# Performance work log

Hardware: AMD Instinct MI355X
Metric: run time of the kernel (lower is better)

The kernel has to match this reference:

```python
import jax, jax.numpy as jnp
import numpy as np

NUM_CLS = 80
C = 256
IMG = 1024.0
N = 256
SR = 2  # sampling_ratio
MIN_SIZE = 16.0
SCALES = (0.25, 0.125, 0.0625, 0.03125)
HW = ((256, 256), (128, 128), (64, 64), (32, 32))


def _roialign(feat, rois, scale, out):
    # feat: [C, H, W]; rois: [n, 4] (y1, x1, y2, x2) in image coords.
    # torchvision-style ROIAlign (aligned=False), sampling_ratio=SR, avg pool.
    Cc, H, W = feat.shape
    n = rois.shape[0]
    y1 = rois[:, 0] * scale
    x1 = rois[:, 1] * scale
    rh = jnp.maximum(rois[:, 2] * scale - y1, 1.0)
    rw = jnp.maximum(rois[:, 3] * scale - x1, 1.0)
    # per-bin sample offsets: (bin + (s+0.5)/SR) * bin_size
    g = (jnp.arange(out, dtype=feat.dtype)[:, None]
         + (jnp.arange(SR, dtype=feat.dtype)[None, :] + 0.5) / SR).reshape(-1)  # [out*SR]
    ys = y1[:, None] + g[None, :] * (rh / out)[:, None]  # [n, out*SR]
    xs = x1[:, None] + g[None, :] * (rw / out)[:, None]
    S = out * SR
    yy = jnp.broadcast_to(ys[:, :, None], (n, S, S)).reshape(n, S * S)
    xx = jnp.broadcast_to(xs[:, None, :], (n, S, S)).reshape(n, S * S)
    valid = (yy > -1.0) & (yy < H) & (xx > -1.0) & (xx < W)
    yc = jnp.clip(yy, 0.0, H - 1.0)
    xc = jnp.clip(xx, 0.0, W - 1.0)
    y0 = jnp.floor(yc)
    x0 = jnp.floor(xc)
    ly = yc - y0
    lx = xc - x0
    y0i = y0.astype(jnp.int32)
    x0i = x0.astype(jnp.int32)
    y1i = jnp.minimum(y0i + 1, H - 1)
    x1i = jnp.minimum(x0i + 1, W - 1)
    f00 = feat[:, y0i, x0i]  # [C, n, S*S]
    f01 = feat[:, y0i, x1i]
    f10 = feat[:, y1i, x0i]
    f11 = feat[:, y1i, x1i]
    val = (f00 * (1 - ly) * (1 - lx) + f01 * (1 - ly) * lx
           + f10 * ly * (1 - lx) + f11 * ly * lx)
    val = jnp.where(valid[None], val, 0.0)
    val = val.reshape(Cc, n, out, SR, out, SR).mean(axis=(3, 5))
    return val.transpose(1, 0, 2, 3)  # [n, C, out, out]


def _pool(P, rois, out):
    # roi_layer: FPN level assignment via log2 of sqrt(area)/224, clamp to levels 0..3
    area = jnp.prod(rois[:, 2:4] - rois[:, 0:2] + 1.0, axis=-1)
    lvl = jnp.clip(jnp.floor(4.0 + jnp.log(jnp.sqrt(area) / 224.0) / np.log(2.0)), 2.0, 5.0) - 2.0
    lvl = lvl.astype(jnp.int32)
    pooled = jnp.zeros((rois.shape[0], C, out, out), dtype=rois.dtype)
    for l in range(4):
        pl = _roialign(P[l], rois, SCALES[l], out)
        pooled = pooled + jnp.where((lvl == l)[:, None, None, None], pl, 0.0)
    return pooled


def _loc2bbox(loc, anchor):
    chw = anchor[..., 2:4] - anchor[..., 0:2]
    cyx = anchor[..., 0:2] + chw * 0.5
    yx = loc[..., 0:2] * chw + cyx
    hw = jnp.exp(loc[..., 2:4]) * chw
    return jnp.concatenate([yx - hw * 0.5, yx + hw * 0.5], axis=-1)


def _head(x, W1, b1, W2, b2, Wc, bc, Wl, bl):
    x = x.reshape(x.shape[0], -1)
    h = jax.nn.relu(x @ W1 + b1)
    h = jax.nn.relu(h @ W2 + b2)
    return h @ Wc + bc, h @ Wl + bl


def _cascade(P, rois, params):
    stds = (jnp.array([0.1, 0.1, 0.2, 0.2], dtype=rois.dtype),
            jnp.array([0.05, 0.05, 0.1, 0.1], dtype=rois.dtype),
            jnp.array([1 / 30.0, 1 / 30.0, 1 / 15.0, 1 / 15.0], dtype=rois.dtype))
    roi = rois
    valid = jnp.ones((rois.shape[0],), dtype=bool)
    t = jnp.arange(rois.shape[0])
    pre_b = jnp.zeros((rois.shape[0], NUM_CLS, 4), dtype=rois.dtype)
    pre_s = jnp.zeros((rois.shape[0], NUM_CLS), dtype=rois.dtype)
    for s in range(3):
        x = _pool(P, roi, 7)
        logits, loc = _head(x, *params[s])
        loc = loc.reshape(-1, NUM_CLS + 1, 4)[:, 1:] * stds[s]
        boxes = _loc2bbox(loc, roi[:, None, :])  # [N, NUM_CLS, 4]
        score = jax.nn.softmax(logits, axis=-1)[:, 1:]
        pre_b = pre_b + boxes
        pre_s = pre_s + score
        best = jnp.argmax(score, axis=-1)
        roi = boxes[t, best]
        roi = jnp.clip(roi, 0.0, IMG)  # square image: clamp both coords to [0, IMG]
        if s < 2:  # original filters only after stages 1 and 2
            hw = roi[:, 2:4] - roi[:, 0:2]
            valid = valid & jnp.all(hw >= MIN_SIZE, axis=-1)
    m = valid.astype(pre_s.dtype)
    return pre_b / 3.0 * m[:, None, None], pre_s / 3.0 * m[:, None]


def setup_inputs():
    key = jax.random.key(0)
    ks = jax.random.split(key, 32)
    inp = {}
    for i, (h, w) in enumerate(HW):
        inp[f"P{i}"] = jax.random.normal(ks[i], (C, h, w), dtype=jnp.float32)
    yx1 = jax.random.uniform(ks[4], (N, 2), minval=0.0, maxval=IMG - 64.0)
    sz = jnp.exp(jax.random.uniform(ks[5], (N, 2), minval=np.log(16.0), maxval=np.log(600.0)))
    yx2 = jnp.clip(yx1 + sz, 0.0, IMG - 1.0)
    inp["rois"] = jnp.concatenate([yx1, yx2], axis=-1).astype(jnp.float32)
    dims = [(C * 49, 1024), (1024,), (1024, 1024), (1024,),
            (1024, NUM_CLS + 1), (NUM_CLS + 1,), (1024, (NUM_CLS + 1) * 4), ((NUM_CLS + 1) * 4,)]
    names = ["W1", "b1", "W2", "b2", "Wc", "bc", "Wl", "bl"]
    k = 6
    for s in range(3):
        for nm, d in zip(names, dims):
            if len(d) == 1:
                inp[f"s{s}_{nm}"] = jnp.zeros(d, dtype=jnp.float32)
            else:
                inp[f"s{s}_{nm}"] = 0.02 * jax.random.normal(ks[k], d, dtype=jnp.float32)
                k += 1
    return inp


def reference(P0, P1, P2, P3, rois,
              s0_W1, s0_b1, s0_W2, s0_b2, s0_Wc, s0_bc, s0_Wl, s0_bl,
              s1_W1, s1_b1, s1_W2, s1_b2, s1_Wc, s1_bc, s1_Wl, s1_bl,
              s2_W1, s2_b1, s2_W2, s2_b2, s2_Wc, s2_bc, s2_Wl, s2_bl):
    P = (P0, P1, P2, P3)
    params = [(s0_W1, s0_b1, s0_W2, s0_b2, s0_Wc, s0_bc, s0_Wl, s0_bl),
              (s1_W1, s1_b1, s1_W2, s1_b2, s1_Wc, s1_bc, s1_Wl, s1_bl),
              (s2_W1, s2_b1, s2_W2, s2_b2, s2_Wc, s2_bc, s2_Wl, s2_bl)]
    return _cascade(P, rois, params)
```

## Files before the change

### kernel.cpp

```cpp
#include <hip/hip_runtime.h>
#include <math.h>


#define NROI 256
#define NCLS 80
#define APITCH 40

typedef __attribute__((ext_vector_type(8))) short short8;
typedef __attribute__((ext_vector_type(4))) float f32x4;

struct __attribute__((aligned(8))) US4 { unsigned short a, b, c, d; };

__device__ __forceinline__ unsigned short f2bf(float f) {
  unsigned u = __builtin_bit_cast(unsigned, f);
  unsigned r = (u + 0x7FFFu + ((u >> 16) & 1u)) >> 16;
  return (unsigned short)r;
}
__device__ __forceinline__ float bf2f(unsigned short u) {
  return __builtin_bit_cast(float, (unsigned)u << 16);
}

struct PrepArgs {
  const float* W1[3];
  const float* W2[3];
  const float* Wc[3];
  const float* Wl[3];
  unsigned short* Wt1[3];
  unsigned short* Wt2[3];
  unsigned short* Wth[3];
  const float* rois;
  float* roi;
  float* valid;
  float* zero_base;
  int zero_count;
};

__global__ __launch_bounds__(256) void prep_all(PrepArgs a) {
  __shared__ unsigned short tile[32][33];
  const int b = blockIdx.x;
  const int t = threadIdx.x;
  const int r = t >> 3;
  const int c4 = (t & 7) * 4;

  if (b < 37632) {
    int s = b / 12544;
    int tau = b % 12544;
    int kd0 = (tau % 392) * 32;
    int n0 = (tau / 392) * 32;
    int p = kd0 >> 8;
    int c0 = kd0 & 255;
    int k_src = (c0 + r) * 49 + p;
    float4 v = *(const float4*)(a.W1[s] + (size_t)k_src * 1024 + n0 + c4);
    tile[r][c4 + 0] = f2bf(v.x);
    tile[r][c4 + 1] = f2bf(v.y);
    tile[r][c4 + 2] = f2bf(v.z);
    tile[r][c4 + 3] = f2bf(v.w);
    __syncthreads();
    US4 o = {tile[c4 + 0][r], tile[c4 + 1][r], tile[c4 + 2][r], tile[c4 + 3][r]};
    *(US4*)(a.Wt1[s] + (size_t)(n0 + r) * 12544 + kd0 + c4) = o;
  } else if (b < 40704) {
    int bb = b - 37632;
    int s = bb / 1024;
    int tau = bb % 1024;
    int k0 = (tau % 32) * 32;
    int n0 = (tau / 32) * 32;
    float4 v = *(const float4*)(a.W2[s] + (size_t)(k0 + r) * 1024 + n0 + c4);
    tile[r][c4 + 0] = f2bf(v.x);
    tile[r][c4 + 1] = f2bf(v.y);
    tile[r][c4 + 2] = f2bf(v.z);
    tile[r][c4 + 3] = f2bf(v.w);
    __syncthreads();
    US4 o = {tile[c4 + 0][r], tile[c4 + 1][r], tile[c4 + 2][r], tile[c4 + 3][r]};
    *(US4*)(a.Wt2[s] + (size_t)(n0 + r) * 1024 + k0 + c4) = o;
  } else if (b < 42240) {
    int bb = b - 40704;
    int s = bb / 512;
    int tau = bb % 512;
    int k0 = (tau % 32) * 32;
    int n0 = (tau / 32) * 32;
#pragma unroll
    for (int j = 0; j < 4; j++) {
      int nn = n0 + c4 + j;
      float v = 0.0f;
      if (nn < 81) v = a.Wc[s][(size_t)(k0 + r) * 81 + nn];
      else if (nn < 405) v = a.Wl[s][(size_t)(k0 + r) * 324 + (nn - 81)];
      tile[r][c4 + j] = f2bf(v);
    }
    __syncthreads();
    US4 o = {tile[c4 + 0][r], tile[c4 + 1][r], tile[c4 + 2][r], tile[c4 + 3][r]};
    *(US4*)(a.Wth[s] + (size_t)(n0 + r) * 1024 + k0 + c4) = o;
  } else if (b == 42240) {
    for (int i = t; i < NROI * 4; i += 256) a.roi[i] = a.rois[i];
    a.valid[t] = 1.0f;
  } else {
    int base = (b - 42241) * 1024 + t;
#pragma unroll
    for (int j = 0; j < 4; j++) {
      int ii = base + j * 256;
      if (ii < a.zero_count) a.zero_base[ii] = 0.0f;
    }
  }
}

__global__ __launch_bounds__(256) void feat_all(
    const float* __restrict__ P0, const float* __restrict__ P1,
    const float* __restrict__ P2, const float* __restrict__ P3,
    unsigned short* __restrict__ Pb0, unsigned short* __restrict__ Pb1,
    unsigned short* __restrict__ Pb2, unsigned short* __restrict__ Pb3) {
  __shared__ unsigned short tile[32][33];
  const int b = blockIdx.x;
  const int t = threadIdx.x;
  const float* src;
  unsigned short* dst;
  int N, tau;
  if (b < 16384)      { src = P0; dst = Pb0; N = 65536; tau = b; }
  else if (b < 20480) { src = P1; dst = Pb1; N = 16384; tau = b - 16384; }
  else if (b < 21504) { src = P2; dst = Pb2; N = 4096;  tau = b - 20480; }
  else                { src = P3; dst = Pb3; N = 1024;  tau = b - 21504; }
  int k0 = (tau & 7) * 32;
  int n0 = (tau >> 3) * 32;
  int r = t >> 3;
  int c4 = (t & 7) * 4;
  float4 v = *(const float4*)(src + (size_t)(k0 + r) * N + n0 + c4);
  tile[r][c4 + 0] = f2bf(v.x);
  tile[r][c4 + 1] = f2bf(v.y);
  tile[r][c4 + 2] = f2bf(v.z);
  tile[r][c4 + 3] = f2bf(v.w);
  __syncthreads();
  US4 o = {tile[c4 + 0][r], tile[c4 + 1][r], tile[c4 + 2][r], tile[c4 + 3][r]};
  *(US4*)(dst + (size_t)(n0 + r) * 256 + k0 + c4) = o;
}

__global__ __launch_bounds__(256) void pool_kernel2(
    const unsigned short* __restrict__ Pb0, const unsigned short* __restrict__ Pb1,
    const unsigned short* __restrict__ Pb2, const unsigned short* __restrict__ Pb3,
    const float* __restrict__ roi, unsigned short* __restrict__ pooled) {
  int t = threadIdx.x;
  int n = blockIdx.y;
  int p = blockIdx.x * 4 + (t >> 6);
  if (p >= 49) return;
  int lane = t & 63;
  int c4 = lane * 4;
  int py = p / 7, px = p % 7;

  float r0 = roi[n * 4 + 0];
  float r1 = roi[n * 4 + 1];
  float r2 = roi[n * 4 + 2];
  float r3 = roi[n * 4 + 3];

  float area = (r2 - r0 + 1.0f) * (r3 - r1 + 1.0f);
  float lf = floorf(4.0f + log2f(sqrtf(area) / 224.0f));
  lf = fminf(fmaxf(lf, 2.0f), 5.0f);
  int lvl = (int)lf - 2;

  float scale;
  int H;
  const unsigned short* fb;
  if (lvl == 0)      { scale = 0.25f;    H = 256; fb = Pb0; }
  else if (lvl == 1) { scale = 0.125f;   H = 128; fb = Pb1; }
  else if (lvl == 2) { scale = 0.0625f;  H = 64;  fb = Pb2; }
  else               { scale = 0.03125f; H = 32;  fb = Pb3; }
  int W = H;

  float y1 = r0 * scale;
  float x1 = r1 * scale;
  float rh = fmaxf(r2 * scale - y1, 1.0f);
  float rw = fmaxf(r3 * scale - x1, 1.0f);
  float bh = rh * (1.0f / 7.0f);
  float bw = rw * (1.0f / 7.0f);

  float a0 = 0.f, a1 = 0.f, a2 = 0.f, a3 = 0.f;
#pragma unroll
  for (int ry = 0; ry < 2; ry++) {
    float yy = y1 + ((float)py + ((float)ry + 0.5f) * 0.5f) * bh;
    bool vy = (yy > -1.0f) && (yy < (float)H);
    float ycl = fminf(fmaxf(yy, 0.0f), (float)(H - 1));
    float y0f = floorf(ycl);
    float ly = ycl - y0f;
    int y0i = (int)y0f;
    int y1i = min(y0i + 1, H - 1);
#pragma unroll
    for (int rx = 0; rx < 2; rx++) {
      float xx = x1 + ((float)px + ((float)rx + 0.5f) * 0.5f) * bw;
      bool vx = (xx > -1.0f) && (xx < (float)W);
      float xcl = fminf(fmaxf(xx, 0.0f), (float)(W - 1));
      float x0f = floorf(xcl);
      float lx = xcl - x0f;
      int x0i = (int)x0f;
      int x1i = min(x0i + 1, W - 1);
      float w00 = (1.f - ly) * (1.f - lx);
      float w01 = (1.f - ly) * lx;
      float w10 = ly * (1.f - lx);
      float w11 = ly * lx;
      if (!(vy && vx)) { w00 = w01 = w10 = w11 = 0.f; }
      ushort4 f00 = *(const ushort4*)(fb + ((size_t)(y0i * W + x0i) * 256 + c4));
      ushort4 f01 = *(const ushort4*)(fb + ((size_t)(y0i * W + x1i) * 256 + c4));
      ushort4 f10 = *(const ushort4*)(fb + ((size_t)(y1i * W + x0i) * 256 + c4));
      ushort4 f11 = *(const ushort4*)(fb + ((size_t)(y1i * W + x1i) * 256 + c4));
      a0 += bf2f(f00.x) * w00 + bf2f(f01.x) * w01 + bf2f(f10.x) * w10 + bf2f(f11.x) * w11;
      a1 += bf2f(f00.y) * w00 + bf2f(f01.y) * w01 + bf2f(f10.y) * w10 + bf2f(f11.y) * w11;
      a2 += bf2f(f00.z) * w00 + bf2f(f01.z) * w01 + bf2f(f10.z) * w10 + bf2f(f11.z) * w11;
      a3 += bf2f(f00.w) * w00 + bf2f(f01.w) * w01 + bf2f(f10.w) * w10 + bf2f(f11.w) * w11;
    }
  }
  ushort4 o;
  o.x = f2bf(a0 * 0.25f);
  o.y = f2bf(a1 * 0.25f);
  o.z = f2bf(a2 * 0.25f);
  o.w = f2bf(a3 * 0.25f);
  *(ushort4*)(pooled + (size_t)n * 12544 + p * 256 + c4) = o;
}

__global__ __launch_bounds__(256) void gemm_bf16(
    const unsigned short* __restrict__ A, const unsigned short* __restrict__ B,
    float* __restrict__ Cpart, int M, int N, int K, int iters,
    const float* __restrict__ bias, unsigned short* __restrict__ fused_out) {
  __shared__ unsigned short As[128 * APITCH];
  __shared__ unsigned short Bs[128 * APITCH];
  const int t = threadIdx.x;
  const int n0 = blockIdx.x * 128;
  const int m0 = blockIdx.y * 128;
  const size_t kt0 = (size_t)blockIdx.z * iters * 32;

  const int row = t >> 2;
  const int off = (t & 3) * 8;
  const unsigned short* pa0 = A + (size_t)(m0 + row) * K + kt0 + off;
  const unsigned short* pa1 = pa0 + (size_t)64 * K;
  const unsigned short* pb0 = B + (size_t)(n0 + row) * K + kt0 + off;
  const unsigned short* pb1 = pb0 + (size_t)64 * K;

  const int lane = t & 63;
  const int wave = t >> 6;
  const int wm = (wave >> 1) * 64;
  const int wn = (wave & 1) * 64;
  const int fr = lane & 15;
  const int kq = (lane >> 4) * 8;

  f32x4 acc[4][4];
#pragma unroll
  for (int i = 0; i < 4; i++)
#pragma unroll
    for (int j = 0; j < 4; j++) acc[i][j] = (f32x4){0.f, 0.f, 0.f, 0.f};

  uint4 ra0 = *(const uint4*)pa0;
  uint4 ra1 = *(const uint4*)pa1;
  uint4 rb0 = *(const uint4*)pb0;
  uint4 rb1 = *(const uint4*)pb1;

  for (int it = 0; it < iters; ++it) {
    *(uint4*)&As[row * APITCH + off] = ra0;
    *(uint4*)&As[(row + 64) * APITCH + off] = ra1;
    *(uint4*)&Bs[row * APITCH + off] = rb0;
    *(uint4*)&Bs[(row + 64) * APITCH + off] = rb1;
    __syncthreads();
    if (it + 1 < iters) {
      int d = (it + 1) * 32;
      ra0 = *(const uint4*)(pa0 + d);
      ra1 = *(const uint4*)(pa1 + d);
      rb0 = *(const uint4*)(pb0 + d);
      rb1 = *(const uint4*)(pb1 + d);
    }
    short8 af[4], bfv[4];
#pragma unroll
    for (int f = 0; f < 4; f++)
      af[f] = *(const short8*)&As[(wm + f * 16 + fr) * APITCH + kq];
#pragma unroll
    for (int f = 0; f < 4; f++)
      bfv[f] = *(const short8*)&Bs[(wn + f * 16 + fr) * APITCH + kq];
#pragma unroll
    for (int fm = 0; fm < 4; fm++)
#pragma unroll
      for (int fn = 0; fn < 4; fn++)
        acc[fm][fn] = __builtin_amdgcn_mfma_f32_16x16x32_bf16(af[fm], bfv[fn],
                                                              acc[fm][fn], 0, 0, 0);
    __syncthreads();
  }

  const int colb = n0 + wn + fr;
  const int rowb = m0 + wm + (lane >> 4) * 4;
  if (fused_out) {
#pragma unroll
    for (int fm = 0; fm < 4; fm++)
#pragma unroll
      for (int fn = 0; fn < 4; fn++) {
        int col = colb + fn * 16;
        float bv = bias[col];
#pragma unroll
        for (int r = 0; r < 4; r++) {
          float v = fmaxf(acc[fm][fn][r] + bv, 0.0f);
          fused_out[(size_t)(rowb + fm * 16 + r) * N + col] = f2bf(v);
        }
      }
  } else {
    float* Cp = Cpart + (size_t)blockIdx.z * M * N;
#pragma unroll
    for (int fm = 0; fm < 4; fm++)
#pragma unroll
      for (int fn = 0; fn < 4; fn++)
#pragma unroll
        for (int r = 0; r < 4; r++)
          Cp[(size_t)(rowb + fm * 16 + r) * N + (colb + fn * 16)] = acc[fm][fn][r];
  }
}

__global__ __launch_bounds__(256) void reduce_bias_relu(
    const float* __restrict__ parts, int nparts, const float* __restrict__ bias,
    unsigned short* __restrict__ outb) {
  int i = blockIdx.x * 256 + threadIdx.x;
  float s = 0.0f;
  for (int p = 0; p < nparts; ++p) s += parts[(size_t)p * 262144 + i];
  s = fmaxf(s + bias[i & 1023], 0.0f);
  outb[i] = f2bf(s);
}

__global__ __launch_bounds__(128) void decode_kernel(
    const float* __restrict__ headp, const float* __restrict__ bc,
    const float* __restrict__ bl,
    float* __restrict__ roi, float* __restrict__ valid,
    float* __restrict__ pre_b, float* __restrict__ pre_s,
    float st0, float st1, float st2, float st3, int stage) {
  int n = blockIdx.x;
  int t = threadIdx.x;
  __shared__ float red[128];
  __shared__ int redi[128];
  __shared__ float sroi[4];
  __shared__ float boxes[NCLS][4];

  if (t < 4) sroi[t] = roi[n * 4 + t];
  float l = -INFINITY;
  if (t < 81) {
    float s = 0.f;
#pragma unroll
    for (int z = 0; z < 4; z++) s += headp[(size_t)z * 131072 + n * 512 + t];
    l = s + bc[t];
  }
  red[t] = l;
  __syncthreads();
#pragma unroll
  for (int s = 64; s > 0; s >>= 1) {
    if (t < s) red[t] = fmaxf(red[t], red[t + s]);
    __syncthreads();
  }
  float mx = red[0];
  __syncthreads();
  red[t] = (t < 81) ? expf(l - mx) : 0.0f;
  __syncthreads();
#pragma unroll
  for (int s = 64; s > 0; s >>= 1) {
    if (t < s) red[t] += red[t + s];
    __syncthreads();
  }
  float denom = red[0];
  __syncthreads();

  float score = -INFINITY;
  if (t < NCLS) {
    float lj = 0.f;
#pragma unroll
    for (int z = 0; z < 4; z++) lj += headp[(size_t)z * 131072 + n * 512 + (t + 1)];
    lj += bc[t + 1];
    score = expf(lj - mx) / denom;
    float lp[4];
#pragma unroll
    for (int j = 0; j < 4; j++) {
      float s = 0.f;
#pragma unroll
      for (int z = 0; z < 4; z++)
        s += headp[(size_t)z * 131072 + n * 512 + 81 + (t + 1) * 4 + j];
      lp[j] = s + bl[(t + 1) * 4 + j];
    }
    float dy = lp[0] * st0;
    float dx = lp[1] * st1;
    float dh = lp[2] * st2;
    float dw = lp[3] * st3;
    float h_ = sroi[2] - sroi[0];
    float w_ = sroi[3] - sroi[1];
    float cy = sroi[0] + h_ * 0.5f;
    float cx = sroi[1] + w_ * 0.5f;
    float ny = dy * h_ + cy;
    float nx = dx * w_ + cx;
    float nh = expf(dh) * h_;
    float nw = expf(dw) * w_;
    float b0 = ny - nh * 0.5f;
    float b1v = nx - nw * 0.5f;
    float b2v = ny + nh * 0.5f;
    float b3v = nx + nw * 0.5f;
    int o = (n * NCLS + t) * 4;
    pre_b[o + 0] += b0;
    pre_b[o + 1] += b1v;
    pre_b[o + 2] += b2v;
    pre_b[o + 3] += b3v;
    pre_s[n * NCLS + t] += score;
    boxes[t][0] = b0;
    boxes[t][1] = b1v;
    boxes[t][2] = b2v;
    boxes[t][3] = b3v;
  }
  red[t] = score;
  redi[t] = t;
  __syncthreads();
  for (int s = 64; s > 0; s >>= 1) {
    if (t < s) {
      float o2 = red[t + s];
      int oi = redi[t + s];
      if (o2 > red[t] || (o2 == red[t] && oi < redi[t])) {
        red[t] = o2;
        redi[t] = oi;
      }
    }
    __syncthreads();
  }
  if (t == 0) {
    int best = redi[0];
    float ry1 = fminf(fmaxf(boxes[best][0], 0.0f), 1024.0f);
    float rx1 = fminf(fmaxf(boxes[best][1], 0.0f), 1024.0f);
    float ry2 = fminf(fmaxf(boxes[best][2], 0.0f), 1024.0f);
    float rx2 = fminf(fmaxf(boxes[best][3], 0.0f), 1024.0f);
    roi[n * 4 + 0] = ry1;
    roi[n * 4 + 1] = rx1;
    roi[n * 4 + 2] = ry2;
    roi[n * 4 + 3] = rx2;
    if (stage < 2) {
      float hh = ry2 - ry1, ww = rx2 - rx1;
      if (!(hh >= 16.0f && ww >= 16.0f)) valid[n] = 0.0f;
    }
  }
}

__global__ __launch_bounds__(256) void finalize_kernel(
    const float* __restrict__ pre_b, const float* __restrict__ pre_s,
    const float* __restrict__ valid, float* __restrict__ out) {
  int i = blockIdx.x * 256 + threadIdx.x;
  if (i < NROI * NCLS * 4) {
    int n = i / (NCLS * 4);
    out[i] = pre_b[i] * valid[n] * (1.0f / 3.0f);
  } else if (i < NROI * NCLS * 4 + NROI * NCLS) {
    int j = i - NROI * NCLS * 4;
    int n = j / NCLS;
    out[i] = pre_s[j] * valid[n] * (1.0f / 3.0f);
  }
}

extern "C" void kernel_launch(void* const* d_in, const int* in_sizes, int n_in,
                              void* d_out, int out_size, void* d_ws, size_t ws_size,
                              hipStream_t stream) {
  const float* P0 = (const float*)d_in[0];
  const float* P1 = (const float*)d_in[1];
  const float* P2 = (const float*)d_in[2];
  const float* P3 = (const float*)d_in[3];
  const float* rois = (const float*)d_in[4];
  float* out = (float*)d_out;
  float* ws = (float*)d_ws;

  float* roi   = ws;
  float* valid = roi + 1024;
  float* pre_b = valid + 256;
  float* pre_s = pre_b + 81920;
  float* part1 = pre_s + 20480;
  float* parth = part1 + 14 * 262144;
  unsigned short* pooledb = (unsigned short*)(parth + 4 * 131072);
  unsigned short* Wt1s = pooledb + (size_t)256 * 12544;
  unsigned short* Wt2s = Wt1s + (size_t)3 * 1024 * 12544;
  unsigned short* Wths = Wt2s + (size_t)3 * 1024 * 1024;
  unsigned short* h1b = Wths + (size_t)3 * 512 * 1024;
  unsigned short* h2b = h1b + (size_t)256 * 1024;
  unsigned short* Pb0 = h2b + (size_t)256 * 1024;
  unsigned short* Pb1 = Pb0 + (size_t)65536 * 256;
  unsigned short* Pb2 = Pb1 + (size_t)16384 * 256;
  unsigned short* Pb3 = Pb2 + (size_t)4096 * 256;

  PrepArgs pa;
  for (int s = 0; s < 3; s++) {
    pa.W1[s] = (const float*)d_in[5 + s * 8 + 0];
    pa.W2[s] = (const float*)d_in[5 + s * 8 + 2];
    pa.Wc[s] = (const float*)d_in[5 + s * 8 + 4];
    pa.Wl[s] = (const float*)d_in[5 + s * 8 + 6];
    pa.Wt1[s] = Wt1s + (size_t)s * 1024 * 12544;
    pa.Wt2[s] = Wt2s + (size_t)s * 1024 * 1024;
    pa.Wth[s] = Wths + (size_t)s * 512 * 1024;
  }
  pa.rois = rois;
  pa.roi = roi;
  pa.valid = valid;
  pa.zero_base = pre_b;
  pa.zero_count = 81920 + 20480;

  feat_all<<<21760, 256, 0, stream>>>(P0, P1, P2, P3, Pb0, Pb1, Pb2, Pb3);
  prep_all<<<42341, 256, 0, stream>>>(pa);

  const float stds[3][4] = {
      {0.1f, 0.1f, 0.2f, 0.2f},
      {0.05f, 0.05f, 0.1f, 0.1f},
      {1.0f / 30.0f, 1.0f / 30.0f, 1.0f / 15.0f, 1.0f / 15.0f}};

  for (int s = 0; s < 3; s++) {
    const float* b1 = (const float*)d_in[5 + s * 8 + 1];
    const float* b2 = (const float*)d_in[5 + s * 8 + 3];
    const float* bc = (const float*)d_in[5 + s * 8 + 5];
    const float* bl = (const float*)d_in[5 + s * 8 + 7];

    pool_kernel2<<<dim3(13, 256), 256, 0, stream>>>(Pb0, Pb1, Pb2, Pb3, roi, pooledb);

    gemm_bf16<<<dim3(8, 2, 14), 256, 0, stream>>>(
        pooledb, pa.Wt1[s], part1, 256, 1024, 12544, 28, nullptr, nullptr);
    reduce_bias_relu<<<1024, 256, 0, stream>>>(part1, 14, b1, h1b);

    gemm_bf16<<<dim3(8, 2, 1), 256, 0, stream>>>(
        h1b, pa.Wt2[s], nullptr, 256, 1024, 1024, 32, b2, h2b);

    gemm_bf16<<<dim3(4, 2, 4), 256, 0, stream>>>(
        h2b, pa.Wth[s], parth, 256, 512, 1024, 8, nullptr, nullptr);

    decode_kernel<<<256, 128, 0, stream>>>(parth, bc, bl, roi, valid, pre_b, pre_s,
                                           stds[s][0], stds[s][1], stds[s][2], stds[s][3], s);
  }

  finalize_kernel<<<400, 256, 0, stream>>>(pre_b, pre_s, valid, out);
}
```

Measured before the change: 516.9 us.

## Merge feature/weight transposes into one kernel with larger tiles; split-K second GEMM

Folds the feature-map bf16 transpose into the weight prep kernel and moves from 32x32 to 64x256 tiles. Each thread now writes wide 16-byte rows and launches far fewer blocks, cutting per-block overhead and improving write coalescing. The second FC GEMM changes from a single-slice fused bias/ReLU epilogue running on 16 blocks to an 8-way split-K (128 blocks) followed by a separate reduce kernel. This trades extra partial-sum traffic and one more launch per stage for more parallelism.

```diff
diff --git a/kernel.cpp b/kernel.cpp
--- a/kernel.cpp
+++ b/kernel.cpp
@@ -5,11 +5,10 @@
 #define NROI 256
 #define NCLS 80
 #define APITCH 40
+#define TP 264
 
 typedef __attribute__((ext_vector_type(8))) short short8;
 typedef __attribute__((ext_vector_type(4))) float f32x4;
-
-struct __attribute__((aligned(8))) US4 { unsigned short a, b, c, d; };
 
 __device__ __forceinline__ unsigned short f2bf(float f) {
   unsigned u = __builtin_bit_cast(unsigned, f);
@@ -28,6 +27,8 @@
   unsigned short* Wt1[3];
   unsigned short* Wt2[3];
   unsigned short* Wth[3];
+  const float* P[4];
+  unsigned short* Pb[4];
   const float* rois;
   float* roi;
   float* valid;
@@ -36,99 +37,111 @@
 };
 
 __global__ __launch_bounds__(256) void prep_all(PrepArgs a) {
-  __shared__ unsigned short tile[32][33];
+  __shared__ unsigned short tile[64 * TP];
   const int b = blockIdx.x;
   const int t = threadIdx.x;
-  const int r = t >> 3;
-  const int c4 = (t & 7) * 4;
-
-  if (b < 37632) {
-    int s = b / 12544;
-    int tau = b % 12544;
-    int kd0 = (tau % 392) * 32;
-    int n0 = (tau / 392) * 32;
-    int p = kd0 >> 8;
-    int c0 = kd0 & 255;
-    int k_src = (c0 + r) * 49 + p;
-    float4 v = *(const float4*)(a.W1[s] + (size_t)k_src * 1024 + n0 + c4);
-    tile[r][c4 + 0] = f2bf(v.x);
-    tile[r][c4 + 1] = f2bf(v.y);
-    tile[r][c4 + 2] = f2bf(v.z);
-    tile[r][c4 + 3] = f2bf(v.w);
-    __syncthreads();
-    US4 o = {tile[c4 + 0][r], tile[c4 + 1][r], tile[c4 + 2][r], tile[c4 + 3][r]};
-    *(US4*)(a.Wt1[s] + (size_t)(n0 + r) * 12544 + kd0 + c4) = o;
-  } else if (b < 40704) {
-    int bb = b - 37632;
-    int s = bb / 1024;
-    int tau = bb % 1024;
-    int k0 = (tau % 32) * 32;
-    int n0 = (tau / 32) * 32;
-    float4 v = *(const float4*)(a.W2[s] + (size_t)(k0 + r) * 1024 + n0 + c4);
-    tile[r][c4 + 0] = f2bf(v.x);
-    tile[r][c4 + 1] = f2bf(v.y);
-    tile[r][c4 + 2] = f2bf(v.z);
-    tile[r][c4 + 3] = f2bf(v.w);
-    __syncthreads();
-    US4 o = {tile[c4 + 0][r], tile[c4 + 1][r], tile[c4 + 2][r], tile[c4 + 3][r]};
-    *(US4*)(a.Wt2[s] + (size_t)(n0 + r) * 1024 + k0 + c4) = o;
-  } else if (b < 42240) {
-    int bb = b - 40704;
-    int s = bb / 512;
-    int tau = bb % 512;
-    int k0 = (tau % 32) * 32;
-    int n0 = (tau / 32) * 32;
-#pragma unroll
-    for (int j = 0; j < 4; j++) {
-      int nn = n0 + c4 + j;
-      float v = 0.0f;
-      if (nn < 81) v = a.Wc[s][(size_t)(k0 + r) * 81 + nn];
-      else if (nn < 405) v = a.Wl[s][(size_t)(k0 + r) * 324 + (nn - 81)];
-      tile[r][c4 + j] = f2bf(v);
-    }
-    __syncthreads();
-    US4 o = {tile[c4 + 0][r], tile[c4 + 1][r], tile[c4 + 2][r], tile[c4 + 3][r]};
-    *(US4*)(a.Wth[s] + (size_t)(n0 + r) * 1024 + k0 + c4) = o;
-  } else if (b == 42240) {
+
+  const float* src = nullptr;
+  unsigned short* dst = nullptr;
+  size_t srcN = 0, dstP = 0;
+  int k0 = 0, n0 = 0;
+  int mode = 0;
+  int hs = 0;
+
+  if (b < 2352) {
+    int s = b / 784, tau = b % 784;
+    int kd0 = (tau % 196) * 64;
+    n0 = (tau / 196) * 256;
+    src = a.W1[s]; srcN = 1024;
+    dst = a.Wt1[s]; dstP = 12544;
+    k0 = kd0; mode = 1;
+  } else if (b < 3712) {
+    int x = b - 2352;
+    int l, base;
+    if (x < 1024)      { l = 0; base = x; }
+    else if (x < 1280) { l = 1; base = x - 1024; }
+    else if (x < 1344) { l = 2; base = x - 1280; }
+    else               { l = 3; base = x - 1344; }
+    static const int NHW[4] = {65536, 16384, 4096, 1024};
+    src = a.P[l]; srcN = NHW[l];
+    dst = a.Pb[l]; dstP = 256;
+    k0 = (base & 3) * 64;
+    n0 = (base >> 2) * 256;
+  } else if (b < 3904) {
+    int x = b - 3712;
+    int s = x / 64, tau = x % 64;
+    src = a.W2[s]; srcN = 1024;
+    dst = a.Wt2[s]; dstP = 1024;
+    k0 = (tau % 16) * 64;
+    n0 = (tau / 16) * 256;
+  } else if (b < 4000) {
+    int x = b - 3904;
+    hs = x / 32;
+    int tau = x % 32;
+    dst = a.Wth[hs]; dstP = 1024;
+    k0 = (tau % 16) * 64;
+    n0 = (tau / 16) * 256;
+    mode = 2;
+  } else if (b == 4000) {
     for (int i = t; i < NROI * 4; i += 256) a.roi[i] = a.rois[i];
     a.valid[t] = 1.0f;
+    return;
   } else {
-    int base = (b - 42241) * 1024 + t;
+    int base = (b - 4001) * 1024 + t;
 #pragma unroll
     for (int j = 0; j < 4; j++) {
       int ii = base + j * 256;
       if (ii < a.zero_count) a.zero_base[ii] = 0.0f;
     }
-  }
-}
-
-__global__ __launch_bounds__(256) void feat_all(
-    const float* __restrict__ P0, const float* __restrict__ P1,
-    const float* __restrict__ P2, const float* __restrict__ P3,
-    unsigned short* __restrict__ Pb0, unsigned short* __restrict__ Pb1,
-    unsigned short* __restrict__ Pb2, unsigned short* __restrict__ Pb3) {
-  __shared__ unsigned short tile[32][33];
-  const int b = blockIdx.x;
-  const int t = threadIdx.x;
-  const float* src;
-  unsigned short* dst;
-  int N, tau;
-  if (b < 16384)      { src = P0; dst = Pb0; N = 65536; tau = b; }
-  else if (b < 20480) { src = P1; dst = Pb1; N = 16384; tau = b - 16384; }
-  else if (b < 21504) { src = P2; dst = Pb2; N = 4096;  tau = b - 20480; }
-  else                { src = P3; dst = Pb3; N = 1024;  tau = b - 21504; }
-  int k0 = (tau & 7) * 32;
-  int n0 = (tau >> 3) * 32;
-  int r = t >> 3;
-  int c4 = (t & 7) * 4;
-  float4 v = *(const float4*)(src + (size_t)(k0 + r) * N + n0 + c4);
-  tile[r][c4 + 0] = f2bf(v.x);
-  tile[r][c4 + 1] = f2bf(v.y);
-  tile[r][c4 + 2] = f2bf(v.z);
-  tile[r][c4 + 3] = f2bf(v.w);
+    return;
+  }
+
+  const int rp = t >> 6;
+  const int c4 = (t & 63) * 4;
+  if (mode == 2) {
+#pragma unroll 4
+    for (int pass = 0; pass < 16; pass++) {
+      int r = pass * 4 + rp;
+      int k = k0 + r;
+      unsigned short vv[4];
+#pragma unroll
+      for (int j = 0; j < 4; j++) {
+        int nn = n0 + c4 + j;
+        float v = 0.0f;
+        if (nn < 81) v = a.Wc[hs][(size_t)k * 81 + nn];
+        else if (nn < 405) v = a.Wl[hs][(size_t)k * 324 + (nn - 81)];
+        vv[j] = f2bf(v);
+      }
+      *(uint2*)&tile[r * TP + c4] =
+          (uint2){(unsigned)vv[0] | ((unsigned)vv[1] << 16),
+                  (unsigned)vv[2] | ((unsigned)vv[3] << 16)};
+    }
+  } else {
+    const int p_ = k0 >> 8;
+    const int c0_ = k0 & 255;
+#pragma unroll 4
+    for (int pass = 0; pass < 16; pass++) {
+      int r = pass * 4 + rp;
+      size_t ksrc = (mode == 1) ? ((size_t)(c0_ + r) * 49 + p_) : (size_t)(k0 + r);
+      float4 v = *(const float4*)(src + ksrc * srcN + n0 + c4);
+      *(uint2*)&tile[r * TP + c4] =
+          (uint2){(unsigned)f2bf(v.x) | ((unsigned)f2bf(v.y) << 16),
+                  (unsigned)f2bf(v.z) | ((unsigned)f2bf(v.w) << 16)};
+    }
+  }
   __syncthreads();
-  US4 o = {tile[c4 + 0][r], tile[c4 + 1][r], tile[c4 + 2][r], tile[c4 + 3][r]};
-  *(US4*)(dst + (size_t)(n0 + r) * 256 + k0 + c4) = o;
+
+  unsigned w[32];
+#pragma unroll
+  for (int i = 0; i < 32; i++) {
+    unsigned lo = tile[(2 * i) * TP + t];
+    unsigned hi = tile[(2 * i + 1) * TP + t];
+    w[i] = lo | (hi << 16);
+  }
+  unsigned short* dp = dst + (size_t)(n0 + t) * dstP + k0;
+#pragma unroll
+  for (int j = 0; j < 8; j++)
+    *(uint4*)(dp + j * 8) = (uint4){w[4 * j], w[4 * j + 1], w[4 * j + 2], w[4 * j + 3]};
 }
 
 __global__ __launch_bounds__(256) void pool_kernel2(
@@ -213,8 +226,7 @@
 
 __global__ __launch_bounds__(256) void gemm_bf16(
     const unsigned short* __restrict__ A, const unsigned short* __restrict__ B,
-    float* __restrict__ Cpart, int M, int N, int K, int iters,
-    const float* __restrict__ bias, unsigned short* __restrict__ fused_out) {
+    float* __restrict__ Cpart, int M, int N, int K, int iters) {
   __shared__ unsigned short As[128 * APITCH];
   __shared__ unsigned short Bs[128 * APITCH];
   const int t = threadIdx.x;
@@ -276,31 +288,16 @@
     __syncthreads();
   }
 
+  float* Cp = Cpart + (size_t)blockIdx.z * M * N;
   const int colb = n0 + wn + fr;
   const int rowb = m0 + wm + (lane >> 4) * 4;
-  if (fused_out) {
-#pragma unroll
-    for (int fm = 0; fm < 4; fm++)
-#pragma unroll
-      for (int fn = 0; fn < 4; fn++) {
-        int col = colb + fn * 16;
-        float bv = bias[col];
-#pragma unroll
-        for (int r = 0; r < 4; r++) {
-          float v = fmaxf(acc[fm][fn][r] + bv, 0.0f);
-          fused_out[(size_t)(rowb + fm * 16 + r) * N + col] = f2bf(v);
-        }
-      }
-  } else {
-    float* Cp = Cpart + (size_t)blockIdx.z * M * N;
-#pragma unroll
-    for (int fm = 0; fm < 4; fm++)
-#pragma unroll
-      for (int fn = 0; fn < 4; fn++)
-#pragma unroll
-        for (int r = 0; r < 4; r++)
-          Cp[(size_t)(rowb + fm * 16 + r) * N + (colb + fn * 16)] = acc[fm][fn][r];
-  }
+#pragma unroll
+  for (int fm = 0; fm < 4; fm++)
+#pragma unroll
+    for (int fn = 0; fn < 4; fn++)
+#pragma unroll
+      for (int r = 0; r < 4; r++)
+        Cp[(size_t)(rowb + fm * 16 + r) * N + (colb + fn * 16)] = acc[fm][fn][r];
 }
 
 __global__ __launch_bounds__(256) void reduce_bias_relu(
@@ -457,7 +454,8 @@
   float* pre_b = valid + 256;
   float* pre_s = pre_b + 81920;
   float* part1 = pre_s + 20480;
-  float* parth = part1 + 14 * 262144;
+  float* part2 = part1 + 14 * 262144;
+  float* parth = part2 + 8 * 262144;
   unsigned short* pooledb = (unsigned short*)(parth + 4 * 131072);
   unsigned short* Wt1s = pooledb + (size_t)256 * 12544;
   unsigned short* Wt2s = Wt1s + (size_t)3 * 1024 * 12544;
@@ -479,14 +477,15 @@
     pa.Wt2[s] = Wt2s + (size_t)s * 1024 * 1024;
     pa.Wth[s] = Wths + (size_t)s * 512 * 1024;
   }
+  pa.P[0] = P0; pa.P[1] = P1; pa.P[2] = P2; pa.P[3] = P3;
+  pa.Pb[0] = Pb0; pa.Pb[1] = Pb1; pa.Pb[2] = Pb2; pa.Pb[3] = Pb3;
   pa.rois = rois;
   pa.roi = roi;
   pa.valid = valid;
   pa.zero_base = pre_b;
   pa.zero_count = 81920 + 20480;
 
-  feat_all<<<21760, 256, 0, stream>>>(P0, P1, P2, P3, Pb0, Pb1, Pb2, Pb3);
-  prep_all<<<42341, 256, 0, stream>>>(pa);
+  prep_all<<<4101, 256, 0, stream>>>(pa);
 
   const float stds[3][4] = {
       {0.1f, 0.1f, 0.2f, 0.2f},
@@ -502,14 +501,15 @@
     pool_kernel2<<<dim3(13, 256), 256, 0, stream>>>(Pb0, Pb1, Pb2, Pb3, roi, pooledb);
 
     gemm_bf16<<<dim3(8, 2, 14), 256, 0, stream>>>(
-        pooledb, pa.Wt1[s], part1, 256, 1024, 12544, 28, nullptr, nullptr);
+        pooledb, pa.Wt1[s], part1, 256, 1024, 12544, 28);
     reduce_bias_relu<<<1024, 256, 0, stream>>>(part1, 14, b1, h1b);
 
-    gemm_bf16<<<dim3(8, 2, 1), 256, 0, stream>>>(
-        h1b, pa.Wt2[s], nullptr, 256, 1024, 1024, 32, b2, h2b);
+    gemm_bf16<<<dim3(8, 2, 8), 256, 0, stream>>>(
+        h1b, pa.Wt2[s], part2, 256, 1024, 1024, 4);
+    reduce_bias_relu<<<1024, 256, 0, stream>>>(part2, 8, b2, h2b);
 
     gemm_bf16<<<dim3(4, 2, 4), 256, 0, stream>>>(
-        h2b, pa.Wth[s], parth, 256, 512, 1024, 8, nullptr, nullptr);
+        h2b, pa.Wth[s], parth, 256, 512, 1024, 8);
 
     decode_kernel<<<256, 128, 0, stream>>>(parth, bc, bl, roi, valid, pre_b, pre_s,
                                            stds[s][0], stds[s][1], stds[s][2], stds[s][3], s);
```

New measurement: 515.5 us. About the same (-0.3%).
